# Performance work log

Measured on AMD Instinct MI355X. Metric: run time of the kernel, lower is better.

Reference implementation:

```python
import jax, jax.numpy as jnp
import numpy as np

B, N, C, H = 16, 800, 1024, 16
NC = 128  # cached KV length from the N==128 pass
HD = C // H


def setup_inputs() -> dict:
    key = jax.random.key(0)
    ks = jax.random.split(key, 9)
    s = 0.02  # init scale for weights
    return {
        "x": jax.random.normal(ks[0], (B, N, C), jnp.float32),
        "xpos": jax.random.normal(ks[1], (B, N, C), jnp.float32),
        "k_t": jax.random.normal(ks[2], (B, NC, C), jnp.float32),
        "v_t": jax.random.normal(ks[3], (B, NC, C), jnp.float32),
        "Wq": jax.random.normal(ks[4], (C, C), jnp.float32) * s,
        "Wk": jax.random.normal(ks[5], (C, C), jnp.float32) * s,
        "Wv": jax.random.normal(ks[6], (C, C), jnp.float32) * s,
        "Wp": jax.random.normal(ks[7], (C, C), jnp.float32) * s,
        "bp": jnp.zeros((C,), jnp.float32),
    }


def reference(x, xpos, k_t, v_t, Wq, Wk, Wv, Wp, bp):
    # N == 800 branch: q from x+xpos; k/v concat cached k_t/v_t before projection.
    b, n, c = x.shape
    scale = HD ** -0.5

    q = (x + xpos) @ Wq.T                              # [B, N, C]
    k_in = jnp.concatenate([x + xpos, k_t], axis=1)    # [B, N+NC, C]
    v_in = jnp.concatenate([x, v_t], axis=1)           # [B, N+NC, C]
    k = k_in @ Wk.T
    v = v_in @ Wv.T

    def heads(t):
        return t.reshape(b, t.shape[1], H, HD).transpose(0, 2, 1, 3)  # [B,H,L,HD]

    qh, kh, vh = heads(q), heads(k), heads(v)
    attn = jax.nn.softmax(jnp.einsum('bhqd,bhkd->bhqk', qh, kh) * scale, axis=-1)
    out = jnp.einsum('bhqk,bhkd->bhqd', attn, vh)       # [B,H,N,HD]
    out = out.transpose(0, 2, 1, 3).reshape(b, n, c)
    return out @ Wp.T + bp
```

## Files before the change

kernel.cpp:

```cpp
#include <hip/hip_runtime.h>
#include <hip/hip_bf16.h>

#define NB 16
#define NN 800
#define NCACHE 128
#define NL 928
#define CC 1024
#define NH 16
#define HD 64

typedef __attribute__((ext_vector_type(8))) short bf16x8;
typedef __attribute__((ext_vector_type(4))) float f32x4;
typedef __attribute__((ext_vector_type(2))) __bf16 bf2;

__device__ __forceinline__ short f2bf(float x) {
  union { float f; unsigned u; } c; c.f = x;
  unsigned r = c.u + 0x7fffu + ((c.u >> 16) & 1u);
  return (short)(r >> 16);
}

#define GLD_LDS(gp, lp) __builtin_amdgcn_global_load_lds( \
    (__attribute__((address_space(1))) void*)(gp),        \
    (__attribute__((address_space(3))) void*)(lp), 16, 0, 0)

#define BAR() asm volatile("s_barrier" ::: "memory")
#define SCHEDB() __builtin_amdgcn_sched_barrier(0)

__global__ __launch_bounds__(256) void prep_kv(
    const float* __restrict__ x, const float* __restrict__ xpos,
    const float* __restrict__ ktc, const float* __restrict__ vtc,
    short* __restrict__ k_in, short* __restrict__ v_in) {
  int idx = blockIdx.x * 256 + threadIdx.x;
  int chunk = idx & 127;
  int row = idx >> 7;
  int b = row / NL;
  int lr = row - b * NL;
  int c = chunk * 8;
  float vk[8], vv[8];
  if (lr < NN) {
    const float4* px = (const float4*)(x + ((size_t)(b * NN + lr) * CC + c));
    const float4* pp = (const float4*)(xpos + ((size_t)(b * NN + lr) * CC + c));
    float4 x0 = px[0], x1 = px[1], p0 = pp[0], p1 = pp[1];
    vv[0]=x0.x; vv[1]=x0.y; vv[2]=x0.z; vv[3]=x0.w;
    vv[4]=x1.x; vv[5]=x1.y; vv[6]=x1.z; vv[7]=x1.w;
    vk[0]=x0.x+p0.x; vk[1]=x0.y+p0.y; vk[2]=x0.z+p0.z; vk[3]=x0.w+p0.w;
    vk[4]=x1.x+p1.x; vk[5]=x1.y+p1.y; vk[6]=x1.z+p1.z; vk[7]=x1.w+p1.w;
  } else {
    const float4* pk = (const float4*)(ktc + ((size_t)(b * NCACHE + lr - NN) * CC + c));
    const float4* pv = (const float4*)(vtc + ((size_t)(b * NCACHE + lr - NN) * CC + c));
    float4 k0 = pk[0], k1 = pk[1], v0 = pv[0], v1 = pv[1];
    vk[0]=k0.x; vk[1]=k0.y; vk[2]=k0.z; vk[3]=k0.w;
    vk[4]=k1.x; vk[5]=k1.y; vk[6]=k1.z; vk[7]=k1.w;
    vv[0]=v0.x; vv[1]=v0.y; vv[2]=v0.z; vv[3]=v0.w;
    vv[4]=v1.x; vv[5]=v1.y; vv[6]=v1.z; vv[7]=v1.w;
  }
  bf16x8 ok, ov;
#pragma unroll
  for (int i = 0; i < 8; ++i) { ok[i] = f2bf(vk[i]); ov[i] = f2bf(vv[i]); }
  *(bf16x8*)(k_in + (size_t)row * CC + c) = ok;
  *(bf16x8*)(v_in + (size_t)row * CC + c) = ov;
}

__global__ __launch_bounds__(256) void prep_w(
    const float* __restrict__ Wq, const float* __restrict__ Wk,
    const float* __restrict__ Wv, const float* __restrict__ Wp,
    short* __restrict__ wout) {
  int idx = blockIdx.x * 256 + threadIdx.x;
  int wsel = idx >> 17;
  int off = (idx & 131071) * 8;
  const float* src = wsel == 0 ? Wq : wsel == 1 ? Wk : wsel == 2 ? Wv : Wp;
  float sc = wsel == 0 ? 0.18033688011112042f : 1.0f;
  const float4* p = (const float4*)(src + off);
  float4 a = p[0], b = p[1];
  bf16x8 o;
  o[0]=f2bf(a.x*sc); o[1]=f2bf(a.y*sc); o[2]=f2bf(a.z*sc); o[3]=f2bf(a.w*sc);
  o[4]=f2bf(b.x*sc); o[5]=f2bf(b.y*sc); o[6]=f2bf(b.z*sc); o[7]=f2bf(b.w*sc);
  *(bf16x8*)(wout + (size_t)wsel * 1048576 + off) = o;
}

#define READ_A(QR) \
  _Pragma("unroll") \
  for (int fr = 0; fr < 4; ++fr) \
    _Pragma("unroll") \
    for (int ks = 0; ks < 2; ++ks) \
      af[fr][ks] = *(const bf16x8*)&lds[abase + (QR)*4096 + fr*1024 + (ks ? xk1 : xk0)];

#define READ_B(QC) \
  _Pragma("unroll") \
  for (int fc = 0; fc < 2; ++fc) \
    _Pragma("unroll") \
    for (int ks = 0; ks < 2; ++ks) \
      bfv[(QC)*2+fc][ks] = *(const bf16x8*)&lds[bbase + (QC)*2048 + fc*1024 + (ks ? xk1 : xk0)];

#define MFMA_QUAD(QR, QC) \
  SCHEDB(); __builtin_amdgcn_s_setprio(1); \
  _Pragma("unroll") \
  for (int fr = 0; fr < 4; ++fr) \
    _Pragma("unroll") \
    for (int fc = 0; fc < 2; ++fc) \
      _Pragma("unroll") \
      for (int ks = 0; ks < 2; ++ks) \
        acc[(QR)*4+fr][(QC)*2+fc] = __builtin_amdgcn_mfma_f32_16x16x32_bf16( \
            af[fr][ks], bfv[(QC)*2+fc][ks], acc[(QR)*4+fr][(QC)*2+fc], 0, 0, 0); \
  __builtin_amdgcn_s_setprio(0); SCHEDB()

template<int MODE>
__global__ __launch_bounds__(512, 2) void gemm256(
    const short* __restrict__ A, const short* __restrict__ Bw,
    short* __restrict__ o0, short* __restrict__ o1,
    float* __restrict__ of, const float* __restrict__ bias) {
  __shared__ short lds[65536];
  const int tid = threadIdx.x;
  const int w = tid >> 6, l = tid & 63;
  const int wm = w >> 2, wn = w & 3;
  const int c = l & 15, g2 = l >> 4;
  const int BNT = (MODE == 2) ? 8 : 4;
  const int cpx = gridDim.x >> 3;
  const int swz = (blockIdx.x & 7) * cpx + (blockIdx.x >> 3);
  const int bm = swz / BNT, bn = swz % BNT;
  const int m0 = bm * 256, n0 = bn * 256;

  const int R0 = tid >> 3;
  const int gc0 = (tid & 7) ^ (R0 & 7);
  const short* As_ = A + (size_t)(m0 + R0) * CC + gc0 * 8;
  const short* Bs_ = Bw + (size_t)(n0 + R0) * CC + gc0 * 8;
  const int wofs = w * 512;

#define STAGE_HT(slot, src) do { \
    GLD_LDS((src), &lds[(slot) + wofs]); \
    GLD_LDS((src) + 64 * CC, &lds[(slot) + 4096 + wofs]); } while (0)

  const int xk0 = ((g2) ^ (c & 7)) * 8;
  const int xk1 = ((g2 + 4) ^ (c & 7)) * 8;

  f32x4 acc[8][4] = {};

  STAGE_HT(0,        As_);
  STAGE_HT(8192,     As_ + 128 * CC);
  STAGE_HT(16384,    Bs_);
  STAGE_HT(24576,    Bs_ + 128 * CC);
  STAGE_HT(32768,       As_ + 64);
  STAGE_HT(32768+8192,  As_ + 64 + 128 * CC);
  STAGE_HT(32768+16384, Bs_ + 64);
  STAGE_HT(32768+24576, Bs_ + 64 + 128 * CC);
  asm volatile("s_waitcnt vmcnt(8)" ::: "memory");
  BAR();

#pragma unroll 1
  for (int t = 0; t < 16; ++t) {
    const int pb = (t & 1) << 15;
    const int abase = pb + wm * 8192 + c * 64;
    const int bbase = pb + 16384 + ((wn >> 1) << 13) + ((wn & 1) * 64 + c) * 64;
    bf16x8 af[4][2], bfv[4][2];
    READ_A(0);
    READ_B(0);
    BAR();
    MFMA_QUAD(0, 0);
    BAR();
    READ_B(1);
    BAR();
    MFMA_QUAD(0, 1);
    BAR();
    READ_A(1);
    if (t < 14) {
      const short* bs2 = Bs_ + (t + 2) * 64;
      STAGE_HT(pb + 16384, bs2);
      STAGE_HT(pb + 24576, bs2 + 128 * CC);
    }
    BAR();
    MFMA_QUAD(1, 0);
    BAR();
    if (t < 14) {
      const short* as2 = As_ + (t + 2) * 64;
      STAGE_HT(pb, as2);
      STAGE_HT(pb + 8192, as2 + 128 * CC);
      asm volatile("s_waitcnt vmcnt(8)" ::: "memory");
    } else if (t == 14) {
      asm volatile("s_waitcnt vmcnt(0)" ::: "memory");
    }
    BAR();
    MFMA_QUAD(1, 1);
    BAR();
  }

#pragma unroll
  for (int fr = 0; fr < 8; ++fr)
#pragma unroll
    for (int fc = 0; fc < 4; ++fc) {
      const int row = m0 + wm * 128 + fr * 16 + g2 * 4;
      const int colw = wn * 64 + fc * 16 + c;
      if (MODE == 1) {
        const int col = n0 + colw;
        const float bv = bias[col];
#pragma unroll
        for (int j = 0; j < 4; ++j)
          of[(size_t)(row + j) * CC + col] = acc[fr][fc][j] + bv;
      } else if (MODE == 2) {
        const int col2 = n0 + colw;
        short* base = (col2 < 1024) ? o0 : o1;
        const int col = col2 & 1023;
#pragma unroll
        for (int j = 0; j < 4; ++j)
          base[(size_t)(row + j) * CC + col] = f2bf(acc[fr][fc][j]);
      } else {
        const int col = n0 + colw;
        const int b = row / NL;
        const int rb = row - b * NL;
        const int vtrow = (b * NH + (col >> 6)) * HD + (col & 63);
        ushort4 pk4;
        pk4.x = (unsigned short)f2bf(acc[fr][fc][0]);
        pk4.y = (unsigned short)f2bf(acc[fr][fc][1]);
        pk4.z = (unsigned short)f2bf(acc[fr][fc][2]);
        pk4.w = (unsigned short)f2bf(acc[fr][fc][3]);
        *(ushort4*)(o0 + (size_t)vtrow * NL + rb) = pk4;
      }
    }
}

__global__ __launch_bounds__(256, 4) void attn_fwd(
    const short* __restrict__ qb, const short* __restrict__ kbuf,
    const short* __restrict__ vtb, short* __restrict__ ob) {
  __shared__ short smem[2][4096];
  const int tid = threadIdx.x;
  const int w = tid >> 6;
  const int l = tid & 63;
  const int c = l & 15, g = l >> 4;
  const int swzb = (blockIdx.x & 7) * 224 + (blockIdx.x >> 3);
  const int bh = swzb / 7;
  const int blk7 = swzb - bh * 7;
  const int h = bh & 15, b = bh >> 4;
  const int q0 = blk7 * 128 + w * 32;
  const bool active = q0 < NN;

  const int u = l >> 3;
  const int lK = 8 * w + u;
  const int b16 = lK & 15;
  const int rpK = 8 * (b16 >> 2) + (b16 & 3) + 4 * (lK >> 4);
  const int xK = (l & 7) ^ u;
  const short* srcK = kbuf + (size_t)b * NL * CC + (size_t)rpK * CC + h * HD + xK * 8;
  const int dV = 16 * w + (l >> 2);
  const int xV = (l & 3) ^ ((l >> 3) & 3);
  const short* srcV = vtb + (size_t)bh * HD * NL + (size_t)dV * NL + xV * 8;

  bf16x8 qf[2][2];
  if (active) {
#pragma unroll
    for (int f = 0; f < 2; ++f) {
      const short* qrow = qb + ((size_t)(b * NL + q0 + f * 16 + c) * CC + h * HD + g * 8);
      qf[f][0] = *(const bf16x8*)qrow;
      qf[f][1] = *(const bf16x8*)(qrow + 32);
    }
  }

  const int koff0 = c * 64 + ((g ^ (c & 7)) << 3);
  const int koff1 = c * 64 + (((g + 4) ^ (c & 7)) << 3);
  const int voffb = 2048 + c * 32 + ((g ^ ((c >> 1) & 3)) << 3);

  f32x4 acc[2][4] = {};
  f32x4 ellv[2] = {};

  GLD_LDS(srcK, &smem[0][w * 512]);
  GLD_LDS(srcV, &smem[0][2048 + w * 512]);
  __syncthreads();

  int buf = 0;
  for (int t = 0; t < 29; ++t) {
    if (t < 28) {
      GLD_LDS(srcK + (size_t)(t + 1) * 32 * CC, &smem[buf ^ 1][w * 512]);
      GLD_LDS(srcV + (t + 1) * 32, &smem[buf ^ 1][2048 + w * 512]);
    }
    if (active) {
      const short* S = smem[buf];
      bf16x8 kd0 = *(const bf16x8*)(S + koff0);
      bf16x8 kd1 = *(const bf16x8*)(S + koff1);
      bf16x8 kd2 = *(const bf16x8*)(S + koff0 + 1024);
      bf16x8 kd3 = *(const bf16x8*)(S + koff1 + 1024);
      bf16x8 vf0 = *(const bf16x8*)(S + voffb);
      bf16x8 vf1 = *(const bf16x8*)(S + voffb + 512);
      bf16x8 vf2 = *(const bf16x8*)(S + voffb + 1024);
      bf16x8 vf3 = *(const bf16x8*)(S + voffb + 1536);
      __builtin_amdgcn_s_setprio(1);
#pragma unroll
      for (int f = 0; f < 2; ++f) {
        f32x4 z = {0.f, 0.f, 0.f, 0.f};
        f32x4 s0 = __builtin_amdgcn_mfma_f32_16x16x32_bf16(kd0, qf[f][0], z, 0, 0, 0);
        s0 = __builtin_amdgcn_mfma_f32_16x16x32_bf16(kd1, qf[f][1], s0, 0, 0, 0);
        f32x4 s1 = __builtin_amdgcn_mfma_f32_16x16x32_bf16(kd2, qf[f][0], z, 0, 0, 0);
        s1 = __builtin_amdgcn_mfma_f32_16x16x32_bf16(kd3, qf[f][1], s1, 0, 0, 0);
        f32x4 e0, e1;
        e0[0] = __builtin_amdgcn_exp2f(s0[0]);
        e0[1] = __builtin_amdgcn_exp2f(s0[1]);
        e0[2] = __builtin_amdgcn_exp2f(s0[2]);
        e0[3] = __builtin_amdgcn_exp2f(s0[3]);
        e1[0] = __builtin_amdgcn_exp2f(s1[0]);
        e1[1] = __builtin_amdgcn_exp2f(s1[1]);
        e1[2] = __builtin_amdgcn_exp2f(s1[2]);
        e1[3] = __builtin_amdgcn_exp2f(s1[3]);
        ellv[f] += e0 + e1;
        union { bf2 h2[4]; bf16x8 v; } pu;
        pu.h2[0] = bf2{(__bf16)e0[0], (__bf16)e0[1]};
        pu.h2[1] = bf2{(__bf16)e0[2], (__bf16)e0[3]};
        pu.h2[2] = bf2{(__bf16)e1[0], (__bf16)e1[1]};
        pu.h2[3] = bf2{(__bf16)e1[2], (__bf16)e1[3]};
        acc[f][0] = __builtin_amdgcn_mfma_f32_16x16x32_bf16(pu.v, vf0, acc[f][0], 0, 0, 0);
        acc[f][1] = __builtin_amdgcn_mfma_f32_16x16x32_bf16(pu.v, vf1, acc[f][1], 0, 0, 0);
        acc[f][2] = __builtin_amdgcn_mfma_f32_16x16x32_bf16(pu.v, vf2, acc[f][2], 0, 0, 0);
        acc[f][3] = __builtin_amdgcn_mfma_f32_16x16x32_bf16(pu.v, vf3, acc[f][3], 0, 0, 0);
      }
      __builtin_amdgcn_s_setprio(0);
    }
    __syncthreads();
    buf ^= 1;
  }

  if (active) {
    float rinv[2];
#pragma unroll
    for (int f = 0; f < 2; ++f) {
      float e = (ellv[f][0] + ellv[f][1]) + (ellv[f][2] + ellv[f][3]);
      e += __shfl_xor(e, 16);
      e += __shfl_xor(e, 32);
      rinv[f] = 1.0f / e;
    }
#pragma unroll
    for (int f = 0; f < 2; ++f) {
      float rj[4];
#pragma unroll
      for (int j = 0; j < 4; ++j) rj[j] = __shfl(rinv[f], g * 4 + j);
      short* orow = ob + (size_t)(b * NN + q0 + f * 16 + g * 4) * CC + h * HD + c;
#pragma unroll
      for (int n = 0; n < 4; ++n)
#pragma unroll
        for (int j = 0; j < 4; ++j)
          orow[(size_t)j * CC + n * 16] = f2bf(acc[f][n][j] * rj[j]);
    }
  }
}

extern "C" void kernel_launch(void* const* d_in, const int* in_sizes, int n_in,
                              void* d_out, int out_size, void* d_ws, size_t ws_size,
                              hipStream_t stream) {
  const float* x    = (const float*)d_in[0];
  const float* xpos = (const float*)d_in[1];
  const float* k_t  = (const float*)d_in[2];
  const float* v_t  = (const float*)d_in[3];
  const float* Wq   = (const float*)d_in[4];
  const float* Wk   = (const float*)d_in[5];
  const float* Wv   = (const float*)d_in[6];
  const float* Wp   = (const float*)d_in[7];
  const float* bp   = (const float*)d_in[8];
  float* out = (float*)d_out;

  char* ws = (char*)d_ws;
  short* k_in = (short*)ws;
  short* v_in = (short*)(ws + 30408704);
  short* wqb  = (short*)(ws + 60817408);
  short* wvb  = (short*)(ws + 65011712);
  short* wpb  = (short*)(ws + 67108864);
  short* qbuf = (short*)(ws + 69206016);
  short* kbuf = (short*)(ws + 99614720);
  short* vtb  = (short*)(ws + 130023424);
  short* attn_o = k_in;

  prep_kv<<<7424, 256, 0, stream>>>(x, xpos, k_t, v_t, k_in, v_in);
  prep_w<<<2048, 256, 0, stream>>>(Wq, Wk, Wv, Wp, wqb);
  gemm256<2><<<464, 512, 0, stream>>>(k_in, wqb, qbuf, kbuf, nullptr, nullptr);
  gemm256<3><<<232, 512, 0, stream>>>(v_in, wvb, vtb, nullptr, nullptr, nullptr);
  attn_fwd<<<1792, 256, 0, stream>>>(qbuf, kbuf, vtb, attn_o);
  gemm256<1><<<200, 512, 0, stream>>>(attn_o, wpb, nullptr, nullptr, out, bp);
}
```

Before: 248.0 us.

## Simplify GEMM main loop to plain double-buffer with two barriers per tile

Replaces the fine-grained 8-barrier interleaved schedule (quadrant MFMAs with sched_barriers and staggered half-tile prefetch two steps ahead) with a simple double-buffered loop. Each iteration prefetches the whole next K-tile into the other buffer, waits, barriers once, reads all of B plus A in two halves, and runs the MFMAs. It drops the sched_barrier pinning so the compiler can interleave LDS reads and MFMAs. This cuts barrier count but shortens the prefetch distance to one tile and raises register pressure from the extra A fragments, which could expose global load latency.

```diff
diff --git a/kernel.cpp b/kernel.cpp
--- a/kernel.cpp
+++ b/kernel.cpp
@@ -24,7 +24,6 @@
     (__attribute__((address_space(3))) void*)(lp), 16, 0, 0)
 
 #define BAR() asm volatile("s_barrier" ::: "memory")
-#define SCHEDB() __builtin_amdgcn_sched_barrier(0)
 
 __global__ __launch_bounds__(256) void prep_kv(
     const float* __restrict__ x, const float* __restrict__ xpos,
@@ -78,31 +77,29 @@
   *(bf16x8*)(wout + (size_t)wsel * 1048576 + off) = o;
 }
 
-#define READ_A(QR) \
+#define READ_A8(dst, QR) \
   _Pragma("unroll") \
   for (int fr = 0; fr < 4; ++fr) \
     _Pragma("unroll") \
     for (int ks = 0; ks < 2; ++ks) \
-      af[fr][ks] = *(const bf16x8*)&lds[abase + (QR)*4096 + fr*1024 + (ks ? xk1 : xk0)];
-
-#define READ_B(QC) \
+      dst[fr][ks] = *(const bf16x8*)&lds[abase + (QR)*4096 + fr*1024 + (ks ? xk1 : xk0)];
+
+#define READ_B8() \
   _Pragma("unroll") \
-  for (int fc = 0; fc < 2; ++fc) \
+  for (int q = 0; q < 4; ++q) \
     _Pragma("unroll") \
     for (int ks = 0; ks < 2; ++ks) \
-      bfv[(QC)*2+fc][ks] = *(const bf16x8*)&lds[bbase + (QC)*2048 + fc*1024 + (ks ? xk1 : xk0)];
-
-#define MFMA_QUAD(QR, QC) \
-  SCHEDB(); __builtin_amdgcn_s_setprio(1); \
+      bfv[q][ks] = *(const bf16x8*)&lds[bbase + q*1024 + (ks ? xk1 : xk0)];
+
+#define MFMA_HALF(QR, asrc) \
   _Pragma("unroll") \
   for (int fr = 0; fr < 4; ++fr) \
     _Pragma("unroll") \
-    for (int fc = 0; fc < 2; ++fc) \
+    for (int fc = 0; fc < 4; ++fc) \
       _Pragma("unroll") \
       for (int ks = 0; ks < 2; ++ks) \
-        acc[(QR)*4+fr][(QC)*2+fc] = __builtin_amdgcn_mfma_f32_16x16x32_bf16( \
-            af[fr][ks], bfv[(QC)*2+fc][ks], acc[(QR)*4+fr][(QC)*2+fc], 0, 0, 0); \
-  __builtin_amdgcn_s_setprio(0); SCHEDB()
+        acc[(QR)*4+fr][fc] = __builtin_amdgcn_mfma_f32_16x16x32_bf16( \
+            asrc[fr][ks], bfv[fc][ks], acc[(QR)*4+fr][fc], 0, 0, 0);
 
 template<int MODE>
 __global__ __launch_bounds__(512, 2) void gemm256(
@@ -135,51 +132,39 @@
 
   f32x4 acc[8][4] = {};
 
-  STAGE_HT(0,        As_);
-  STAGE_HT(8192,     As_ + 128 * CC);
-  STAGE_HT(16384,    Bs_);
-  STAGE_HT(24576,    Bs_ + 128 * CC);
-  STAGE_HT(32768,       As_ + 64);
-  STAGE_HT(32768+8192,  As_ + 64 + 128 * CC);
-  STAGE_HT(32768+16384, Bs_ + 64);
-  STAGE_HT(32768+24576, Bs_ + 64 + 128 * CC);
-  asm volatile("s_waitcnt vmcnt(8)" ::: "memory");
-  BAR();
+  STAGE_HT(0,     As_);
+  STAGE_HT(8192,  As_ + 128 * CC);
+  STAGE_HT(16384, Bs_);
+  STAGE_HT(24576, Bs_ + 128 * CC);
 
 #pragma unroll 1
   for (int t = 0; t < 16; ++t) {
     const int pb = (t & 1) << 15;
+    const int pn = pb ^ 32768;
+    if (t < 15) {
+      const short* as1 = As_ + (t + 1) * 64;
+      const short* bs1 = Bs_ + (t + 1) * 64;
+      STAGE_HT(pn,         as1);
+      STAGE_HT(pn + 8192,  as1 + 128 * CC);
+      STAGE_HT(pn + 16384, bs1);
+      STAGE_HT(pn + 24576, bs1 + 128 * CC);
+      asm volatile("s_waitcnt vmcnt(8)" ::: "memory");
+    } else {
+      asm volatile("s_waitcnt vmcnt(0)" ::: "memory");
+    }
+    BAR();
     const int abase = pb + wm * 8192 + c * 64;
     const int bbase = pb + 16384 + ((wn >> 1) << 13) + ((wn & 1) * 64 + c) * 64;
-    bf16x8 af[4][2], bfv[4][2];
-    READ_A(0);
-    READ_B(0);
-    BAR();
-    MFMA_QUAD(0, 0);
-    BAR();
-    READ_B(1);
-    BAR();
-    MFMA_QUAD(0, 1);
-    BAR();
-    READ_A(1);
-    if (t < 14) {
-      const short* bs2 = Bs_ + (t + 2) * 64;
-      STAGE_HT(pb + 16384, bs2);
-      STAGE_HT(pb + 24576, bs2 + 128 * CC);
-    }
-    BAR();
-    MFMA_QUAD(1, 0);
-    BAR();
-    if (t < 14) {
-      const short* as2 = As_ + (t + 2) * 64;
-      STAGE_HT(pb, as2);
-      STAGE_HT(pb + 8192, as2 + 128 * CC);
-      asm volatile("s_waitcnt vmcnt(8)" ::: "memory");
-    } else if (t == 14) {
-      asm volatile("s_waitcnt vmcnt(0)" ::: "memory");
-    }
-    BAR();
-    MFMA_QUAD(1, 1);
+    bf16x8 afA[4][2], afB[4][2], bfv[4][2];
+    READ_A8(afA, 0);
+    READ_B8();
+    __builtin_amdgcn_s_setprio(1);
+    MFMA_HALF(0, afA);
+    __builtin_amdgcn_s_setprio(0);
+    READ_A8(afB, 1);
+    __builtin_amdgcn_s_setprio(1);
+    MFMA_HALF(1, afB);
+    __builtin_amdgcn_s_setprio(0);
     BAR();
   }
 
```

New measurement: 248.9 us. About the same (+0.3%).
